# Kernel optimization log

Hardware: AMD Instinct MI355X
Metric: run time of the kernel (lower is better)

## Reference

```python
import jax, jax.numpy as jnp
import numpy as np
import math

B, S = 32, 2048
D_MODEL, D_STATE = 1024, 256
DT_MIN, DT_MAX = 1e-3, 0.1
LN_EPS = 1e-5


def setup_inputs() -> dict:
    key = jax.random.key(0)
    k_x, k_b, k_c = jax.random.split(key, 3)
    x = jax.random.normal(k_x, (B, S, D_MODEL), dtype=jnp.float32)
    log_lambda_real = jnp.linspace(math.log(DT_MIN), math.log(DT_MAX), D_STATE).astype(jnp.float32)
    log_b = jax.random.uniform(k_b, (D_STATE, 1), minval=-0.5, maxval=0.5, dtype=jnp.float32)
    c = jax.random.normal(k_c, (1, D_STATE), dtype=jnp.float32) / math.sqrt(D_STATE)
    log_d = jnp.zeros((1,), jnp.float32)
    log_step = jnp.asarray(math.log(DT_MIN), jnp.float32)
    alpha = jnp.asarray(0.7, jnp.float32)
    ln_gamma = jnp.ones((D_STATE,), jnp.float32)
    ln_beta = jnp.zeros((D_STATE,), jnp.float32)
    return {
        "x": x,
        "log_lambda_real": log_lambda_real,
        "log_b": log_b,
        "c": c,
        "log_d": log_d,
        "log_step": log_step,
        "alpha": alpha,
        "ln_gamma": ln_gamma,
        "ln_beta": ln_beta,
    }


def _layer_norm(h, gamma, beta):
    mu = jnp.mean(h, axis=-1, keepdims=True)
    var = jnp.mean((h - mu) ** 2, axis=-1, keepdims=True)
    return (h - mu) * jax.lax.rsqrt(var + LN_EPS) * gamma + beta


def reference(x, log_lambda_real, log_b, c, log_d, log_step, alpha, ln_gamma, ln_beta):
    lam = -jnp.exp(log_lambda_real)          # [N]
    b = jnp.exp(log_b)[:, 0]                 # [N]
    d = jnp.exp(log_d)                       # [1]
    step = jnp.exp(log_step)                 # scalar
    # bilinear discretization
    a_disc = (2.0 + step * lam) / (2.0 - step * lam)        # [N]
    b_disc = step * (1.0 + a_disc) * b / 2.0                 # [N]

    u = jnp.mean(x, axis=-1)                 # [B, S] per-timestep scalar drive
    c_row = c[0]                             # [N]

    def scan_step(h, u_t):
        # h: [B, N], u_t: [B]
        h = a_disc[None, :] * h + b_disc[None, :] * u_t[:, None]
        h = _layer_norm(h, ln_gamma, ln_beta)
        s = h @ c_row                        # [B]
        return h, s

    h0 = jnp.zeros((x.shape[0], a_disc.shape[0]), x.dtype)
    _, s = jax.lax.scan(scan_step, h0, u.T)  # s: [S, B]
    y = s.T[:, :, None] + d * x              # [B, S, D] (broadcast of scalar readout)
    a_sig = jax.nn.sigmoid(alpha)
    return a_sig * x + (1.0 - a_sig) * y
```

## Files before the change

### kernel.cpp

```cpp
#include <hip/hip_runtime.h>

constexpr int B = 32, S = 2048, D = 1024, N = 256;

#define DEV __device__ __forceinline__

template <int CTRL>
DEV float dpp_add(float x) {
  int y = __builtin_amdgcn_update_dpp(0, __float_as_int(x), CTRL, 0xF, 0xF, true);
  return x + __int_as_float(y);
}

DEV float rdlane(float v, int l) {
  return __int_as_float(__builtin_amdgcn_readlane(__float_as_int(v), l));
}

DEV void wave_reduce3(float& a, float& b, float& c) {
  a = dpp_add<0x111>(a); b = dpp_add<0x111>(b); c = dpp_add<0x111>(c);
  a = dpp_add<0x112>(a); b = dpp_add<0x112>(b); c = dpp_add<0x112>(c);
  a = dpp_add<0x114>(a); b = dpp_add<0x114>(b); c = dpp_add<0x114>(c);
  a = dpp_add<0x118>(a); b = dpp_add<0x118>(b); c = dpp_add<0x118>(c);
  a = dpp_add<0x142>(a); b = dpp_add<0x142>(b); c = dpp_add<0x142>(c);
  a = dpp_add<0x143>(a); b = dpp_add<0x143>(b); c = dpp_add<0x143>(c);
  a = rdlane(a, 63);
  b = rdlane(b, 63);
  c = rdlane(c, 63);
}

__global__ __launch_bounds__(256) void mean_kernel(const float4* __restrict__ x4,
                                                   float* __restrict__ u) {
  const int row  = (blockIdx.x << 2) | (threadIdx.x >> 6);
  const int lane = threadIdx.x & 63;
  const float4* xr = x4 + (size_t)row * (D / 4);
  float s = 0.f;
#pragma unroll
  for (int j = 0; j < 4; ++j) {
    float4 v = xr[lane + (j << 6)];
    s += (v.x + v.y) + (v.z + v.w);
  }
#pragma unroll
  for (int off = 32; off; off >>= 1) s += __shfl_xor(s, off, 64);
  if (lane == 0) u[row] = s * (1.f / 1024.f);
}

__global__ __launch_bounds__(64) void scan_kernel(
    const float* __restrict__ u, const float* __restrict__ llr,
    const float* __restrict__ logb, const float* __restrict__ c,
    const float* __restrict__ lstep, const float* __restrict__ gma,
    const float* __restrict__ bta, float* __restrict__ sout) {
  const int b    = blockIdx.x;
  const int lane = threadIdx.x;
  const float stp = expf(lstep[0]);

  float ag[4], ab[4], bd[4], cg[4];
  float Gp = 0.f, BCp = 0.f, d0 = 0.f;
#pragma unroll
  for (int k = 0; k < 4; ++k) {
    const int n = (k << 6) | lane;
    const float lam = -expf(llr[n]);
    const float sl  = stp * lam;
    const float adisc = (2.f + sl) / (2.f - sl);
    const float bdisc = stp * (1.f + adisc) * expf(logb[n]) * 0.5f;
    const float g  = gma[n];
    const float be = bta[n];
    const float cc = c[n];
    ag[k] = adisc * g;
    ab[k] = adisc * be;
    bd[k] = bdisc;
    cg[k] = cc * g;
    Gp  += cg[k];
    BCp += cc * be;
  }
  wave_reduce3(Gp, BCp, d0);
  const float G = Gp, BC = BCp;
  const float Ceps = 65536.f * 1e-5f;

  const float* urow = u + b * S;
  float* srow = sout + b * S;

  float uch = urow[lane];
  const float u0 = rdlane(uch, 0);
  float z0 = bd[0] * u0, z1 = bd[1] * u0, z2 = bd[2] * u0, z3 = bd[3] * u0;

  for (int t0 = 0; t0 < S; t0 += 64) {
    int nx = t0 + 64 + lane;
    if (nx > S - 1) nx = S - 1;
    const float uch_next = urow[nx];
    float stk = 0.f;
#pragma unroll
    for (int tt = 0; tt < 64; ++tt) {
      float s1 = (z0 + z1) + (z2 + z3);
      float s2 = fmaf(z0, z0, z1 * z1) + fmaf(z2, z2, z3 * z3);
      float s3 = fmaf(z0, cg[0], z1 * cg[1]) + fmaf(z2, cg[2], z3 * cg[3]);
      wave_reduce3(s1, s2, s3);
      const float q = fmaf(256.f, s2, fmaf(-s1, s1, Ceps));
      const float r = __builtin_amdgcn_rsqf(q);
      const float st = fmaf(r, fmaf(256.f, s3, -s1 * G), BC);
      stk = (lane == tt) ? st : stk;

      const float un = (tt < 63) ? rdlane(uch, tt + 1) : rdlane(uch_next, 0);
      const float w0 = fmaf(256.f, z0, -s1);
      const float w1 = fmaf(256.f, z1, -s1);
      const float w2 = fmaf(256.f, z2, -s1);
      const float w3 = fmaf(256.f, z3, -s1);
      z0 = fmaf(ag[0] * w0, r, fmaf(bd[0], un, ab[0]));
      z1 = fmaf(ag[1] * w1, r, fmaf(bd[1], un, ab[1]));
      z2 = fmaf(ag[2] * w2, r, fmaf(bd[2], un, ab[2]));
      z3 = fmaf(ag[3] * w3, r, fmaf(bd[3], un, ab[3]));
    }
    srow[t0 + lane] = stk;
    uch = uch_next;
  }
}

__global__ __launch_bounds__(256) void out_kernel(
    const float4* __restrict__ x4, const float* __restrict__ s,
    const float* __restrict__ logd, const float* __restrict__ alpha,
    float4* __restrict__ o4) {
  const float asig = 1.f / (1.f + expf(-alpha[0]));
  const float dd   = expf(logd[0]);
  const float cx   = asig + (1.f - asig) * dd;
  const float cs   = 1.f - asig;
  const int i = blockIdx.x * 256 + threadIdx.x;
  const float sv = cs * s[i >> 8];
  const float4 v = x4[i];
  float4 o;
  o.x = fmaf(cx, v.x, sv);
  o.y = fmaf(cx, v.y, sv);
  o.z = fmaf(cx, v.z, sv);
  o.w = fmaf(cx, v.w, sv);
  o4[i] = o;
}

extern "C" void kernel_launch(void* const* d_in, const int* in_sizes, int n_in,
                              void* d_out, int out_size, void* d_ws, size_t ws_size,
                              hipStream_t stream) {
  const float* x     = (const float*)d_in[0];
  const float* llr   = (const float*)d_in[1];
  const float* logb  = (const float*)d_in[2];
  const float* c     = (const float*)d_in[3];
  const float* logd  = (const float*)d_in[4];
  const float* lstep = (const float*)d_in[5];
  const float* alpha = (const float*)d_in[6];
  const float* gma   = (const float*)d_in[7];
  const float* bta   = (const float*)d_in[8];

  float* u = (float*)d_ws;
  float* s = u + B * S;

  mean_kernel<<<B * S / 4, 256, 0, stream>>>((const float4*)x, u);
  scan_kernel<<<B, 64, 0, stream>>>(u, llr, logb, c, lstep, gma, bta, s);
  out_kernel<<<(B * S * D / 4) / 256, 256, 0, stream>>>(
      (const float4*)x, s, logd, alpha, (float4*)d_out);
}
```

Measured before the change: 692.1 us.

## Fuse scan and output into one kernel with flag-based chunk pipelining

Merges the sequential scan and the elementwise output pass into a single launch. 32 blocks run the per-batch scan with raised priority and publish each 64-step chunk of readouts through a per-batch flag. 128 worker blocks spin on those flags and write the output rows for each chunk as soon as it is ready, so the bandwidth-bound output pass overlaps the latency-bound scan. This adds a flag memset, atomic stores and polling, and it relies on all 160 blocks being co-resident. Worker blocks share the CUs with the scan waves, and each worker processes only 64 rows per chunk.

```diff
diff --git a/kernel.cpp b/kernel.cpp
--- a/kernel.cpp
+++ b/kernel.cpp
@@ -1,6 +1,9 @@
 #include <hip/hip_runtime.h>
 
 constexpr int B = 32, S = 2048, D = 1024, N = 256;
+constexpr int NCHUNK = 32;
+constexpr int SBLK   = 32;
+constexpr int WBLK   = 128;
 
 #define DEV __device__ __forceinline__
 
@@ -26,6 +29,13 @@
   c = rdlane(c, 63);
 }
 
+DEV float ld_agent(const float* p) {
+  return __hip_atomic_load(p, __ATOMIC_RELAXED, __HIP_MEMORY_SCOPE_AGENT);
+}
+DEV int ld_flag(const int* p) {
+  return __hip_atomic_load(p, __ATOMIC_RELAXED, __HIP_MEMORY_SCOPE_AGENT);
+}
+
 __global__ __launch_bounds__(256) void mean_kernel(const float4* __restrict__ x4,
                                                    float* __restrict__ u) {
   const int row  = (blockIdx.x << 2) | (threadIdx.x >> 6);
@@ -42,93 +52,111 @@
   if (lane == 0) u[row] = s * (1.f / 1024.f);
 }
 
-__global__ __launch_bounds__(64) void scan_kernel(
-    const float* __restrict__ u, const float* __restrict__ llr,
+__global__ __launch_bounds__(1024) void fused(
+    const float4* __restrict__ x4, const float* __restrict__ llr,
     const float* __restrict__ logb, const float* __restrict__ c,
     const float* __restrict__ lstep, const float* __restrict__ gma,
-    const float* __restrict__ bta, float* __restrict__ sout) {
-  const int b    = blockIdx.x;
-  const int lane = threadIdx.x;
-  const float stp = expf(lstep[0]);
+    const float* __restrict__ bta, const float* __restrict__ logd,
+    const float* __restrict__ alpha, const float* __restrict__ u,
+    float* __restrict__ s, int* __restrict__ sflag, float4* __restrict__ o4) {
+  const int wv   = threadIdx.x >> 6;
+  const int lane = threadIdx.x & 63;
 
-  float ag[4], ab[4], bd[4], cg[4];
-  float Gp = 0.f, BCp = 0.f, d0 = 0.f;
+  if (blockIdx.x >= SBLK) {
+    const int wb = blockIdx.x - SBLK;
+    const int b  = wb >> 2;
+    const int i  = ((wb & 3) << 4) | wv;
+    const float asig = 1.f / (1.f + expf(-alpha[0]));
+    const float dd   = expf(logd[0]);
+    const float cx   = asig + (1.f - asig) * dd;
+    const float cs   = 1.f - asig;
+    for (int ch = 0; ch < NCHUNK; ++ch) {
+      if (threadIdx.x == 0) {
+        while (ld_flag(&sflag[b << 5]) < ch + 1) __builtin_amdgcn_s_sleep(8);
+      }
+      __syncthreads();
+      const int t = (ch << 6) | i;
+      const float sv = cs * ld_agent(&s[b * S + t]);
+      const float4* xr   = x4 + (size_t)(b * S + t) * (D / 4);
+      float4*       orow = o4 + (size_t)(b * S + t) * (D / 4);
 #pragma unroll
-  for (int k = 0; k < 4; ++k) {
-    const int n = (k << 6) | lane;
-    const float lam = -expf(llr[n]);
-    const float sl  = stp * lam;
-    const float adisc = (2.f + sl) / (2.f - sl);
-    const float bdisc = stp * (1.f + adisc) * expf(logb[n]) * 0.5f;
-    const float g  = gma[n];
-    const float be = bta[n];
-    const float cc = c[n];
-    ag[k] = adisc * g;
-    ab[k] = adisc * be;
-    bd[k] = bdisc;
-    cg[k] = cc * g;
-    Gp  += cg[k];
-    BCp += cc * be;
+      for (int k = 0; k < 4; ++k) {
+        float4 v = xr[lane + (k << 6)];
+        float4 o;
+        o.x = fmaf(cx, v.x, sv);
+        o.y = fmaf(cx, v.y, sv);
+        o.z = fmaf(cx, v.z, sv);
+        o.w = fmaf(cx, v.w, sv);
+        orow[lane + (k << 6)] = o;
+      }
+    }
+  } else if (wv == 0) {
+    const int b = blockIdx.x;
+    __builtin_amdgcn_s_setprio(1);
+    const float stp = expf(lstep[0]);
+
+    float ag[4], ab[4], bd[4], cg[4];
+    float Gp = 0.f, BCp = 0.f, d0 = 0.f;
+#pragma unroll
+    for (int k = 0; k < 4; ++k) {
+      const int n = (k << 6) | lane;
+      const float lam = -expf(llr[n]);
+      const float sl  = stp * lam;
+      const float adisc = (2.f + sl) / (2.f - sl);
+      const float bdisc = stp * (1.f + adisc) * expf(logb[n]) * 0.5f;
+      const float g  = gma[n];
+      const float be = bta[n];
+      const float cc = c[n];
+      ag[k] = adisc * g;
+      ab[k] = adisc * be;
+      bd[k] = bdisc;
+      cg[k] = cc * g;
+      Gp  += cg[k];
+      BCp += cc * be;
+    }
+    wave_reduce3(Gp, BCp, d0);
+    const float G = Gp, BC = BCp;
+    const float Ceps = 65536.f * 1e-5f;
+
+    const float* urow = u + b * S;
+    float* srow = s + b * S;
+
+    float uch = urow[lane];
+    const float u0 = rdlane(uch, 0);
+    float z0 = bd[0] * u0, z1 = bd[1] * u0, z2 = bd[2] * u0, z3 = bd[3] * u0;
+
+    for (int t0 = 0; t0 < S; t0 += 64) {
+      int nx = t0 + 64 + lane;
+      if (nx > S - 1) nx = S - 1;
+      const float uch_next = urow[nx];
+      float stk = 0.f;
+#pragma unroll
+      for (int tt = 0; tt < 64; ++tt) {
+        float s1 = (z0 + z1) + (z2 + z3);
+        float s2 = fmaf(z0, z0, z1 * z1) + fmaf(z2, z2, z3 * z3);
+        float s3 = fmaf(z0, cg[0], z1 * cg[1]) + fmaf(z2, cg[2], z3 * cg[3]);
+        wave_reduce3(s1, s2, s3);
+        const float q = fmaf(256.f, s2, fmaf(-s1, s1, Ceps));
+        const float r = __builtin_amdgcn_rsqf(q);
+        const float st = fmaf(r, fmaf(256.f, s3, -s1 * G), BC);
+        stk = (lane == tt) ? st : stk;
+
+        const float un = (tt < 63) ? rdlane(uch, tt + 1) : rdlane(uch_next, 0);
+        const float w0 = fmaf(256.f, z0, -s1);
+        const float w1 = fmaf(256.f, z1, -s1);
+        const float w2 = fmaf(256.f, z2, -s1);
+        const float w3 = fmaf(256.f, z3, -s1);
+        z0 = fmaf(ag[0] * w0, r, fmaf(bd[0], un, ab[0]));
+        z1 = fmaf(ag[1] * w1, r, fmaf(bd[1], un, ab[1]));
+        z2 = fmaf(ag[2] * w2, r, fmaf(bd[2], un, ab[2]));
+        z3 = fmaf(ag[3] * w3, r, fmaf(bd[3], un, ab[3]));
+      }
+      atomicExch(&srow[t0 + lane], stk);
+      asm volatile("s_waitcnt vmcnt(0)" ::: "memory");
+      if (lane == 0) atomicExch(&sflag[b << 5], (t0 >> 6) + 1);
+      uch = uch_next;
+    }
   }
-  wave_reduce3(Gp, BCp, d0);
-  const float G = Gp, BC = BCp;
-  const float Ceps = 65536.f * 1e-5f;
-
-  const float* urow = u + b * S;
-  float* srow = sout + b * S;
-
-  float uch = urow[lane];
-  const float u0 = rdlane(uch, 0);
-  float z0 = bd[0] * u0, z1 = bd[1] * u0, z2 = bd[2] * u0, z3 = bd[3] * u0;
-
-  for (int t0 = 0; t0 < S; t0 += 64) {
-    int nx = t0 + 64 + lane;
-    if (nx > S - 1) nx = S - 1;
-    const float uch_next = urow[nx];
-    float stk = 0.f;
-#pragma unroll
-    for (int tt = 0; tt < 64; ++tt) {
-      float s1 = (z0 + z1) + (z2 + z3);
-      float s2 = fmaf(z0, z0, z1 * z1) + fmaf(z2, z2, z3 * z3);
-      float s3 = fmaf(z0, cg[0], z1 * cg[1]) + fmaf(z2, cg[2], z3 * cg[3]);
-      wave_reduce3(s1, s2, s3);
-      const float q = fmaf(256.f, s2, fmaf(-s1, s1, Ceps));
-      const float r = __builtin_amdgcn_rsqf(q);
-      const float st = fmaf(r, fmaf(256.f, s3, -s1 * G), BC);
-      stk = (lane == tt) ? st : stk;
-
-      const float un = (tt < 63) ? rdlane(uch, tt + 1) : rdlane(uch_next, 0);
-      const float w0 = fmaf(256.f, z0, -s1);
-      const float w1 = fmaf(256.f, z1, -s1);
-      const float w2 = fmaf(256.f, z2, -s1);
-      const float w3 = fmaf(256.f, z3, -s1);
-      z0 = fmaf(ag[0] * w0, r, fmaf(bd[0], un, ab[0]));
-      z1 = fmaf(ag[1] * w1, r, fmaf(bd[1], un, ab[1]));
-      z2 = fmaf(ag[2] * w2, r, fmaf(bd[2], un, ab[2]));
-      z3 = fmaf(ag[3] * w3, r, fmaf(bd[3], un, ab[3]));
-    }
-    srow[t0 + lane] = stk;
-    uch = uch_next;
-  }
-}
-
-__global__ __launch_bounds__(256) void out_kernel(
-    const float4* __restrict__ x4, const float* __restrict__ s,
-    const float* __restrict__ logd, const float* __restrict__ alpha,
-    float4* __restrict__ o4) {
-  const float asig = 1.f / (1.f + expf(-alpha[0]));
-  const float dd   = expf(logd[0]);
-  const float cx   = asig + (1.f - asig) * dd;
-  const float cs   = 1.f - asig;
-  const int i = blockIdx.x * 256 + threadIdx.x;
-  const float sv = cs * s[i >> 8];
-  const float4 v = x4[i];
-  float4 o;
-  o.x = fmaf(cx, v.x, sv);
-  o.y = fmaf(cx, v.y, sv);
-  o.z = fmaf(cx, v.z, sv);
-  o.w = fmaf(cx, v.w, sv);
-  o4[i] = o;
 }
 
 extern "C" void kernel_launch(void* const* d_in, const int* in_sizes, int n_in,
@@ -144,11 +172,13 @@
   const float* gma   = (const float*)d_in[7];
   const float* bta   = (const float*)d_in[8];
 
-  float* u = (float*)d_ws;
-  float* s = u + B * S;
+  float* u     = (float*)d_ws;
+  float* s     = u + B * S;
+  int*   sflag = (int*)(s + B * S);
 
+  hipMemsetAsync(sflag, 0, B * 32 * sizeof(int), stream);
   mean_kernel<<<B * S / 4, 256, 0, stream>>>((const float4*)x, u);
-  scan_kernel<<<B, 64, 0, stream>>>(u, llr, logb, c, lstep, gma, bta, s);
-  out_kernel<<<(B * S * D / 4) / 256, 256, 0, stream>>>(
-      (const float4*)x, s, logd, alpha, (float4*)d_out);
+  fused<<<SBLK + WBLK, 1024, 0, stream>>>(
+      (const float4*)x, llr, logb, c, lstep, gma, bta, logd, alpha,
+      u, s, sflag, (float4*)d_out);
 }
```

After: 630.1 us. -9.0%, faster.
